# Optimization experiments

Measured on AMD Instinct MI355X. Metric: run time of the kernel, lower is better.

The kernel has to match this reference:

```python
import jax, jax.numpy as jnp
import numpy as np

B, CIN, T = 32, 1024, 600
NES, SCALE = 8, 8
CBLK = CIN // NES          # 128 channels per outer block
W = CBLK // SCALE          # 16 channels per scale branch
NIN = SCALE - 1            # 7 inner conv branches per Bottle2neck
NOUT = NES - 1             # 7 outer Bottle2neck blocks
NCLS = 2
EPS = 1e-5


def _bn1d(x, p):  # x:(B,C,T), p:(4,C) = gamma,beta,running_mean,running_var (inference BN)
    g, b, m, v = p
    return (x - m[:, None]) * (g[:, None] * jax.lax.rsqrt(v[:, None] + EPS)) + b[:, None]


def _bn2d(x, p):  # x:(B,C,T,S), p:(4,C)
    g, b, m, v = p
    r = lambda a: a[:, None, None]
    return (x - r(m)) * (r(g) * jax.lax.rsqrt(r(v) + EPS)) + r(b)


def _conv1x1(x, w, b):  # x:(B,C,T), w:(O,C), b:(O,)
    return jnp.einsum('oc,bct->bot', w, x) + b[:, None]


def _bottle2neck(x, w1, b1, bn1, cw, cb, ibn, ws, w3, b3, bn3, s1w, s1b, s2w, s2b):
    residual = x
    out = _bn1d(jax.nn.relu(_conv1x1(x, w1, b1)), bn1)[..., None]  # (B,128,T,1)
    spx = [out[:, i * W:(i + 1) * W] for i in range(SCALE)]
    sp = spx[NIN]
    outs = []
    for j in range(NIN):
        sp = jnp.concatenate([sp, spx[j]], axis=-1)                # (B,W,T,j+2)
        y = jax.lax.conv_general_dilated(
            sp, cw[j], window_strides=(1, 1), padding=((2, 2), (0, 0)),
            rhs_dilation=(2, 1), dimension_numbers=('NCHW', 'OIHW', 'NCHW'))
        y = y + cb[j][None, :, None, None]
        sp = _bn2d(jax.nn.relu(y), ibn[j])
        outs.append(jnp.sum(sp * ws[j][None, None, None, :], axis=-1))  # learnable weighted sum over scale dim
    outs.append(spx[NIN][..., 0])
    out = jnp.concatenate(outs, axis=1)                            # (B,128,T)
    out = _bn1d(jax.nn.relu(_conv1x1(out, w3, b3)), bn3)
    s = jnp.mean(out, axis=-1, keepdims=True)                      # SE squeeze
    s = jax.nn.relu(jnp.einsum('oc,bcx->box', s1w, s) + s1b[:, None])
    s = jax.nn.sigmoid(jnp.einsum('oc,bcx->box', s2w, s) + s2b[:, None])
    return out * s + residual


def _fwd(x, w1, b1, bn1, cw, cb, ibn, ws0, ws1, ws2, ws3, ws4, ws5, ws6,
         w3, b3, bn3, se1w, se1b, se2w, se2b, obn, fbn, fcw, fcb):
    wss = [ws0, ws1, ws2, ws3, ws4, ws5, ws6]
    spx = [x[:, i * CBLK:(i + 1) * CBLK] for i in range(NES)]
    sp = None
    outs = []
    for i in range(NOUT):
        sp = spx[i] if i == 0 else sp + spx[i]
        sp = _bottle2neck(sp, w1[i], b1[i], bn1[i], cw[i], cb[i], ibn[i],
                          [w[i] for w in wss], w3[i], b3[i], bn3[i],
                          se1w[i], se1b[i], se2w[i], se2b[i])
        sp = _bn1d(jax.nn.relu(sp), obn[i])
        outs.append(sp)
    outs.append(spx[-1])
    out = jax.nn.relu(_bn1d(jnp.concatenate(outs, axis=1), fbn))   # (B,1024,T)
    out = jnp.mean(out, axis=-1)                                   # mean pooling over time
    return out @ fcw.T + fcb                                       # (B,2)


def setup_inputs():
    key = jax.random.key(0)
    keys = iter(jax.random.split(key, 64))
    nrm = lambda shape, s=1.0: s * jax.random.normal(next(keys), shape, jnp.float32)

    def bn_params(shape):
        g = 1.0 + nrm(shape, 0.1)
        b = nrm(shape, 0.1)
        m = nrm(shape, 0.1)
        v = 0.5 + jax.random.uniform(next(keys), shape, jnp.float32)
        return jnp.stack([g, b, m, v], axis=-2)  # (..., 4, C)

    inp = {
        'x': nrm((B, CIN, T)),
        'w1': nrm((NOUT, CBLK, CBLK), CBLK ** -0.5), 'b1': nrm((NOUT, CBLK), 0.02),
        'bn1': bn_params((NOUT, CBLK)),
        'cw': nrm((NOUT, NIN, W, W, 3, 1), (W * 3) ** -0.5), 'cb': nrm((NOUT, NIN, W), 0.02),
        'ibn': bn_params((NOUT, NIN, W)),
        'w3': nrm((NOUT, CBLK, CBLK), CBLK ** -0.5), 'b3': nrm((NOUT, CBLK), 0.02),
        'bn3': bn_params((NOUT, CBLK)),
        'se1w': nrm((NOUT, CBLK // 8, CBLK), CBLK ** -0.5), 'se1b': nrm((NOUT, CBLK // 8), 0.02),
        'se2w': nrm((NOUT, CBLK, CBLK // 8), (CBLK // 8) ** -0.5), 'se2b': nrm((NOUT, CBLK), 0.02),
        'obn': bn_params((NOUT, CBLK)),
        'fbn': bn_params((CIN,)),
        'fcw': nrm((NCLS, CIN), CIN ** -0.5), 'fcb': nrm((NCLS,), 0.02),
    }
    for j in range(NIN):
        inp[f'ws{j}'] = jnp.full((NOUT, j + 2), 1.0 / (j + 2), jnp.float32)
    return inp


def reference(x, w1, b1, bn1, cw, cb, ibn, ws0, ws1, ws2, ws3, ws4, ws5, ws6,
              w3, b3, bn3, se1w, se1b, se2w, se2b, obn, fbn, fcw, fcb):
    return _fwd(x, w1, b1, bn1, cw, cb, ibn, ws0, ws1, ws2, ws3, ws4, ws5, ws6,
                w3, b3, bn3, se1w, se1b, se2w, se2b, obn, fbn, fcw, fcb)
```

## Files before the change

kernel.cpp:

```cpp
#include <hip/hip_runtime.h>
#include <hip/hip_bf16.h>

#define B_ 32
#define T_ 600

typedef __attribute__((ext_vector_type(8))) short short8;
typedef __attribute__((ext_vector_type(4))) float f32x4;
typedef __attribute__((ext_vector_type(4))) unsigned short ushort4v;

static __device__ __forceinline__ unsigned short f2bf(float f) {
    unsigned u = __float_as_uint(f);
    u += 0x7FFFu + ((u >> 16) & 1u);
    return (unsigned short)(u >> 16);
}
static __device__ __forceinline__ float bf2f(unsigned short u) {
    return __uint_as_float(((unsigned)u) << 16);
}

template<bool HAS_IN2, bool DO_SSUM, bool OUT_BF16>
__global__ __launch_bounds__(256) void gemm_kernel(
    const float* __restrict__ in0, int s0,
    const float* __restrict__ in1,
    const float* __restrict__ Wg, const float* __restrict__ bias,
    const float* __restrict__ bnp, void* __restrict__ outv,
    float* __restrict__ ssum,
    float* __restrict__ zbuf4096)
{
    __shared__ unsigned short Al[128][136];
    __shared__ unsigned short Bl[64][136];
    const int tid = threadIdx.x;
    const int b = blockIdx.y;
    const int t0 = blockIdx.x * 64;

    if (zbuf4096 != nullptr) {
        int fid = (b * gridDim.x + blockIdx.x) * 256 + tid;
        if (fid < 4096) zbuf4096[fid] = 0.f;
    }

    for (int e = tid; e < 128 * 32; e += 256) {
        int row = e >> 5, c4 = (e & 31) * 4;
        float4 w4 = *(const float4*)&Wg[row * 128 + c4];
        ushort4v u;
        u.x = f2bf(w4.x); u.y = f2bf(w4.y); u.z = f2bf(w4.z); u.w = f2bf(w4.w);
        *(ushort4v*)&Al[row][c4] = u;
    }
    {
        int t = tid & 63, cb = tid >> 6;
        int gt = t0 + t;
        bool inr = gt < T_;
        const float* p0 = in0 + b * s0 + gt;
        const float* p1 = HAS_IN2 ? (in1 + b * 614400 + gt) : nullptr;
        for (int q = 0; q < 32; q += 8) {
            unsigned short u8[8];
#pragma unroll
            for (int r = 0; r < 8; ++r) {
                int c = cb * 32 + q + r;
                float v = 0.f;
                if (inr) {
                    v = p0[c * T_];
                    if (HAS_IN2) v += p1[c * T_];
                }
                u8[r] = f2bf(v);
            }
            *(short8*)&Bl[t][cb * 32 + q] = *(short8*)u8;
        }
    }
    __syncthreads();

    const int wave = tid >> 6, lane = tid & 63;
    const int mBase = (wave >> 1) * 64, nBase = (wave & 1) * 32;
    const int lr = lane & 15, lq = lane >> 4;

    f32x4 acc[4][2];
#pragma unroll
    for (int mf = 0; mf < 4; ++mf)
#pragma unroll
        for (int nf = 0; nf < 2; ++nf) acc[mf][nf] = {0.f, 0.f, 0.f, 0.f};

#pragma unroll
    for (int kb = 0; kb < 4; ++kb) {
        short8 af[4], bfr[2];
#pragma unroll
        for (int mf = 0; mf < 4; ++mf)
            af[mf] = *(const short8*)&Al[mBase + mf * 16 + lr][kb * 32 + lq * 8];
#pragma unroll
        for (int nf = 0; nf < 2; ++nf)
            bfr[nf] = *(const short8*)&Bl[nBase + nf * 16 + lr][kb * 32 + lq * 8];
#pragma unroll
        for (int mf = 0; mf < 4; ++mf)
#pragma unroll
            for (int nf = 0; nf < 2; ++nf)
                acc[mf][nf] = __builtin_amdgcn_mfma_f32_16x16x32_bf16(
                    af[mf], bfr[nf], acc[mf][nf], 0, 0, 0);
    }

#pragma unroll
    for (int mf = 0; mf < 4; ++mf) {
#pragma unroll
        for (int i = 0; i < 4; ++i) {
            int o = mBase + mf * 16 + lq * 4 + i;
            float g = bnp[o], be = bnp[128 + o], m = bnp[256 + o], vv = bnp[384 + o];
            float sc = g * rsqrtf(vv + 1e-5f), sh = be - m * sc;
            float bs = bias[o];
            float psum = 0.f;
#pragma unroll
            for (int nf = 0; nf < 2; ++nf) {
                int t = t0 + nBase + nf * 16 + lr;
                float v = fmaxf(acc[mf][nf][i] + bs, 0.f) * sc + sh;
                if (t < T_) {
                    if (OUT_BF16)
                        ((unsigned short*)outv)[(b * 128 + o) * T_ + t] = f2bf(v);
                    else
                        ((float*)outv)[(b * 128 + o) * T_ + t] = v;
                    psum += v;
                }
            }
            if (DO_SSUM) {
                psum += __shfl_xor(psum, 1);
                psum += __shfl_xor(psum, 2);
                psum += __shfl_xor(psum, 4);
                psum += __shfl_xor(psum, 8);
                if (lr == 0) atomicAdd(&ssum[b * 128 + o], psum);
            }
        }
    }
}

constexpr int TI = 100;
constexpr int NROW = 132;
constexpr int RS = 24;

__global__ __launch_bounds__(128, 3) void inner_kernel(
    const unsigned short* __restrict__ out1, float* __restrict__ mid,
    unsigned short* __restrict__ chainout,
    const float* __restrict__ cwB, const float* __restrict__ cbB,
    const float* __restrict__ ibnB)
{
    __shared__ __attribute__((aligned(16))) unsigned short st[2][NROW][RS];
    __shared__ __attribute__((aligned(16))) unsigned short wL1[7 * 16 * 32];
    __shared__ __attribute__((aligned(16))) unsigned short wL2[7 * 16 * 16];
    __shared__ __attribute__((aligned(16))) unsigned short zb[16];
    __shared__ __attribute__((aligned(16))) float pL[7 * 16][4];

    const int tid = threadIdx.x;
    const int tile = blockIdx.x;
    const int c = blockIdx.y;
    const int b = blockIdx.z;

    const int j0 = (c <= 1) ? 0 : (c - 1);
    const int nconv = 7 - j0;
    const int halo = 2 * nconv;
    const int X = TI + 2 * halo;
    const int ch0 = (c == 0) ? 112 : 16 * (c - 1);
    const int t0g = tile * TI - halo;

    for (int e = tid; e < 2 * NROW * RS / 4; e += 128)
        ((ushort4v*)st)[e] = ushort4v{0, 0, 0, 0};
    if (tid < 16) zb[tid] = 0;

    for (int e = tid; e < nconv * 512; e += 128) {
        int k = e >> 9, rem = e & 511, o = rem >> 5, col = rem & 31;
        int tap = col >> 4, i = col & 15;
        wL1[e] = f2bf(cwB[((j0 + k) * 16 + o) * 48 + i * 3 + tap]);
    }
    for (int e = tid; e < nconv * 256; e += 128) {
        int k = e >> 8, rem = e & 255, o = rem >> 4, i = rem & 15;
        wL2[e] = f2bf(cwB[((j0 + k) * 16 + o) * 48 + i * 3 + 2]);
    }
    for (int e = tid; e < nconv * 16; e += 128) {
        int k = e >> 4, o = e & 15, j = j0 + k;
        float g = ibnB[(j * 4 + 0) * 16 + o], bb = ibnB[(j * 4 + 1) * 16 + o];
        float m = ibnB[(j * 4 + 2) * 16 + o], v = ibnB[(j * 4 + 3) * 16 + o];
        float sc = g * rsqrtf(v + 1e-5f);
        pL[e][0] = cbB[j * 16 + o];
        pL[e][1] = sc;
        pL[e][2] = bb - m * sc;
        pL[e][3] = 0.f;
    }
    __syncthreads();

    {
        const int i = tid >> 3, ph = tid & 7;
        const unsigned short* src = out1 + (size_t)(b * 128 + ch0 + i) * T_;
        for (int t = ph; t < X; t += 8) {
            int g = t0g + t;
            unsigned short v = ((unsigned)g < (unsigned)T_) ? src[g] : (unsigned short)0;
            st[0][t + 2][i] = v;
            if (c == 0 && t >= halo && t < halo + TI)
                mid[(size_t)(b * 128 + 112 + i) * T_ + g] = bf2f(v);
        }
    }
    __syncthreads();

    const int lane = tid & 63, wave = tid >> 6;
    const int lt = lane & 15, q = lane >> 4;
    const int i0 = (q & 1) * 8;
    const int roff1 = (q < 2) ? 0 : 2;

    int cur = 0;
    for (int k = 0; k < nconv; ++k) {
        const int olo = 2 * k + 2, ohi = X - 2 * k - 2;
        const int thi = (ohi + 15) >> 4;
        const int nxt = cur ^ 1;

        short8 A1 = *(const short8*)&wL1[(k * 16 + lt) * 32 + q * 8];
        short8 A2 = (q < 2)
            ? *(const short8*)&wL2[(k * 16 + lt) * 16 + q * 8]
            : *(const short8*)&zb[i0];
        float4 pp[4];
#pragma unroll
        for (int r = 0; r < 4; ++r)
            pp[r] = *(const float4*)&pL[k * 16 + 4 * q + r][0];

        for (int tt = wave; tt < thi; tt += 2) {
            const int t = tt * 16 + lt;
            f32x4 acc = {0.f, 0.f, 0.f, 0.f};
            short8 B1 = *(const short8*)&st[cur][t + roff1][i0];
            acc = __builtin_amdgcn_mfma_f32_16x16x32_bf16(A1, B1, acc, 0, 0, 0);
            short8 B2 = *(const short8*)&st[cur][t + 4][i0];
            acc = __builtin_amdgcn_mfma_f32_16x16x32_bf16(A2, B2, acc, 0, 0, 0);

            const int g = t0g + t;
            const bool ok = (t >= olo) && (t < ohi) && ((unsigned)g < (unsigned)T_);
            ushort4v o4;
#pragma unroll
            for (int r = 0; r < 4; ++r) {
                float v = fmaxf(acc[r] + pp[r].x, 0.f) * pp[r].y + pp[r].z;
                unsigned short h = f2bf(v);
                o4[r] = ok ? h : (unsigned short)0;
            }
            *(ushort4v*)&st[nxt][t + 2][4 * q] = o4;
        }
        __syncthreads();

        {
            const int j = j0 + k;
            const int pair = j * (j + 3) / 2 + c;
            unsigned short* dst = chainout + ((size_t)(pair * B_ + b) * 16) * T_
                                + tile * TI;
            const int i = tid >> 3, ph = tid & 7;
            for (int t2 = ph; t2 < TI; t2 += 8)
                dst[i * T_ + t2] = st[nxt][halo + t2 + 2][i];
        }
        cur = nxt;
    }
}

constexpr int WSUM_ITEMS = 7 * B_ * 16 * 75;

__global__ __launch_bounds__(256) void wsum_kernel(
    const unsigned short* __restrict__ chainout, float* __restrict__ mid,
    const float* __restrict__ ws0, const float* __restrict__ ws1,
    const float* __restrict__ ws2, const float* __restrict__ ws3,
    const float* __restrict__ ws4, const float* __restrict__ ws5,
    const float* __restrict__ ws6)
{
    int e = blockIdx.x * 256 + threadIdx.x;
    if (e >= WSUM_ITEMS) return;
    const int j = e / (B_ * 16 * 75);
    int r = e - j * (B_ * 16 * 75);
    const int b = r / (16 * 75);
    r -= b * (16 * 75);
    const int i = r / 75;
    const int tv = r - i * 75;

    const float* wp;
    switch (j) {
        case 0: wp = ws0; break; case 1: wp = ws1; break;
        case 2: wp = ws2; break; case 3: wp = ws3; break;
        case 4: wp = ws4; break; case 5: wp = ws5; break;
        default: wp = ws6; break;
    }
    const int nsl = j + 2, pair0 = j * (j + 3) / 2;
    const unsigned short* src = chainout + (size_t)(pair0 * B_ + b) * 9600
                              + i * T_ + tv * 8;
    float acc[8] = {0.f, 0.f, 0.f, 0.f, 0.f, 0.f, 0.f, 0.f};
    for (int s = 0; s < nsl; ++s) {
        short8 v = *(const short8*)(src + (size_t)s * B_ * 9600);
        float w = wp[s];
#pragma unroll
        for (int d = 0; d < 8; ++d)
            acc[d] += w * bf2f((unsigned short)v[d]);
    }
    float* dst = mid + (size_t)(b * 128 + 16 * j + i) * T_ + tv * 8;
    *(f32x4*)dst = {acc[0], acc[1], acc[2], acc[3]};
    *(f32x4*)(dst + 4) = {acc[4], acc[5], acc[6], acc[7]};
}

__global__ __launch_bounds__(128) void se_kernel(
    const float* __restrict__ ssum, const float* __restrict__ w1se,
    const float* __restrict__ b1se, const float* __restrict__ w2se,
    const float* __restrict__ b2se, float* __restrict__ s2b)
{
    __shared__ float sL[128], hL[16];
    const int tid = threadIdx.x, b = blockIdx.x;
    sL[tid] = ssum[b * 128 + tid] * (1.f / 600.f);
    __syncthreads();
    if (tid < 16) {
        float a = b1se[tid];
        for (int c = 0; c < 128; ++c) a += w1se[tid * 128 + c] * sL[c];
        hL[tid] = fmaxf(a, 0.f);
    }
    __syncthreads();
    float a = b2se[tid];
#pragma unroll
    for (int q = 0; q < 16; ++q) a += w2se[tid * 16 + q] * hL[q];
    s2b[b * 128 + tid] = 1.f / (1.f + expf(-a));
}

template<bool HAS_R2>
__global__ __launch_bounds__(256) void fuse_kernel(
    const float* __restrict__ out3, const float* __restrict__ s2b,
    const float* __restrict__ res0, int r0s,
    const float* __restrict__ res1,
    const float* __restrict__ obnp, const float* __restrict__ fbnp, int chOff,
    float* __restrict__ spOut, float* __restrict__ pooled)
{
    const int tid = threadIdx.x;
    const int row = blockIdx.x * 4 + (tid >> 6);
    const int lane = tid & 63;
    const int b = row >> 7, c = row & 127;
    const float s2v = s2b[b * 128 + c];
    float g = obnp[c], bb = obnp[128 + c], m = obnp[256 + c], v = obnp[384 + c];
    float osc = g * rsqrtf(v + 1e-5f), osh = bb - m * osc;
    int fc = chOff + c;
    float fg = fbnp[fc], fb2 = fbnp[1024 + fc], fm = fbnp[2048 + fc], fv = fbnp[3072 + fc];
    float fsc = fg * rsqrtf(fv + 1e-5f), fsh = fb2 - fm * fsc;
    int base = (b * 128 + c) * T_;
    float psum = 0.f;
    for (int t = lane; t < T_; t += 64) {
        float o3 = out3[base + t];
        float r = res0[b * r0s + c * T_ + t];
        if (HAS_R2) r += res1[b * 614400 + c * T_ + t];
        float fin = o3 * s2v + r;
        float sp = fmaxf(fin, 0.f) * osc + osh;
        spOut[base + t] = sp;
        psum += fmaxf(sp * fsc + fsh, 0.f);
    }
    for (int mo = 32; mo > 0; mo >>= 1) psum += __shfl_xor(psum, mo);
    if (lane == 0) pooled[b * 1024 + fc] = psum * (1.f / 600.f);
}

__global__ __launch_bounds__(256) void pooledx_kernel(
    const float* __restrict__ x, const float* __restrict__ fbnp,
    float* __restrict__ pooled)
{
    const int tid = threadIdx.x;
    const int row = blockIdx.x * 4 + (tid >> 6);
    const int lane = tid & 63;
    const int b = row >> 7, c = row & 127;
    int fc = 896 + c;
    float fg = fbnp[fc], fb2 = fbnp[1024 + fc], fm = fbnp[2048 + fc], fv = fbnp[3072 + fc];
    float fsc = fg * rsqrtf(fv + 1e-5f), fsh = fb2 - fm * fsc;
    int base = (b * 1024 + fc) * T_;
    float psum = 0.f;
    for (int t = lane; t < T_; t += 64)
        psum += fmaxf(x[base + t] * fsc + fsh, 0.f);
    for (int mo = 32; mo > 0; mo >>= 1) psum += __shfl_xor(psum, mo);
    if (lane == 0) pooled[b * 1024 + fc] = psum * (1.f / 600.f);
}

__global__ __launch_bounds__(256) void logits_kernel(
    const float* __restrict__ pooled, const float* __restrict__ fcw,
    const float* __restrict__ fcb, float* __restrict__ outp)
{
    __shared__ float red[256];
    const int tid = threadIdx.x;
    const int item = tid & 63, part = tid >> 6;
    const int b = item >> 1, cls = item & 1;
    float a = 0.f;
    for (int c = part * 256; c < part * 256 + 256; ++c)
        a += pooled[b * 1024 + c] * fcw[cls * 1024 + c];
    red[tid] = a;
    __syncthreads();
    if (tid < 64)
        outp[b * 2 + cls] = red[tid] + red[tid + 64] + red[tid + 128] + red[tid + 192] + fcb[cls];
}

extern "C" void kernel_launch(void* const* d_in, const int* in_sizes, int n_in,
                              void* d_out, int out_size, void* d_ws, size_t ws_size,
                              hipStream_t stream) {
    const float* x    = (const float*)d_in[0];
    const float* w1   = (const float*)d_in[1];
    const float* b1   = (const float*)d_in[2];
    const float* bn1  = (const float*)d_in[3];
    const float* cw   = (const float*)d_in[4];
    const float* cb   = (const float*)d_in[5];
    const float* ibn  = (const float*)d_in[6];
    const float* w3   = (const float*)d_in[7];
    const float* b3   = (const float*)d_in[8];
    const float* bn3  = (const float*)d_in[9];
    const float* se1w = (const float*)d_in[10];
    const float* se1b = (const float*)d_in[11];
    const float* se2w = (const float*)d_in[12];
    const float* se2b = (const float*)d_in[13];
    const float* obn  = (const float*)d_in[14];
    const float* fbn  = (const float*)d_in[15];
    const float* fcw  = (const float*)d_in[16];
    const float* fcb  = (const float*)d_in[17];
    const float* wsp[7] = {(const float*)d_in[18], (const float*)d_in[19],
                           (const float*)d_in[20], (const float*)d_in[21],
                           (const float*)d_in[22], (const float*)d_in[23],
                           (const float*)d_in[24]};

    float* ws = (float*)d_ws;
    const int NT = 128 * T_ * B_;
    unsigned short* out1h = (unsigned short*)ws;
    float* mid    = ws + NT;
    float* out3   = mid + NT;
    float* spA    = out3 + NT;
    float* spB    = spA + NT;
    float* sbuf   = spB + NT;
    float* s2b    = sbuf + 7 * 4096;
    float* pooled = s2b + 4096;
    unsigned short* chainout = (unsigned short*)(pooled + 32768);

    pooledx_kernel<<<1024, 256, 0, stream>>>(x, fbn, pooled);

    dim3 gGrid(10, B_);
    dim3 iGrid(6, 8, B_);
    const int wGrid = (WSUM_ITEMS + 255) / 256;

    float* spBufs[2] = {spA, spB};
    for (int i = 0; i < 7; ++i) {
        float* spOut = spBufs[i & 1];
        const float* spIn = spBufs[(i & 1) ^ 1];

        if (i == 0)
            gemm_kernel<false, false, true><<<gGrid, 256, 0, stream>>>(
                x, 614400, nullptr, w1, b1, bn1, out1h, nullptr,
                sbuf + i * 4096);
        else
            gemm_kernel<true, false, true><<<gGrid, 256, 0, stream>>>(
                spIn, 76800, x + i * 76800,
                w1 + i * 16384, b1 + i * 128, bn1 + i * 512, out1h, nullptr,
                sbuf + i * 4096);

        inner_kernel<<<iGrid, 128, 0, stream>>>(
            out1h, mid, chainout, cw + i * 5376, cb + i * 112, ibn + i * 448);

        wsum_kernel<<<wGrid, 256, 0, stream>>>(
            chainout, mid,
            wsp[0] + 2 * i, wsp[1] + 3 * i, wsp[2] + 4 * i, wsp[3] + 5 * i,
            wsp[4] + 6 * i, wsp[5] + 7 * i, wsp[6] + 8 * i);

        gemm_kernel<false, true, false><<<gGrid, 256, 0, stream>>>(
            mid, 76800, nullptr,
            w3 + i * 16384, b3 + i * 128, bn3 + i * 512, out3, sbuf + i * 4096,
            nullptr);

        se_kernel<<<B_, 128, 0, stream>>>(
            sbuf + i * 4096, se1w + i * 2048, se1b + i * 16,
            se2w + i * 2048, se2b + i * 128, s2b);

        if (i == 0)
            fuse_kernel<false><<<1024, 256, 0, stream>>>(
                out3, s2b, x, 614400, nullptr, obn, fbn, 0, spOut, pooled);
        else
            fuse_kernel<true><<<1024, 256, 0, stream>>>(
                out3, s2b, spIn, 76800, x + i * 76800,
                obn + i * 512, fbn, i * 128, spOut, pooled);
    }

    logits_kernel<<<1, 256, 0, stream>>>(pooled, fcw, fcb, (float*)d_out);
}
```

Baseline: 912.2 us.

## Fuse scale-weighted sum into conv3 GEMM and SE into fuse kernel; halve inner tile

The separate weighted-sum kernel and its fp32 'mid' buffer are removed. The second 1x1 GEMM now builds its B tile directly from the bf16 chain outputs, applying the learnable scale weights, and reads the passthrough channels from out1h. The SE excitation MLP moves into every fuse block, replacing the se_kernel launch, and the inner conv tile shrinks from 100 to 50 timesteps to double the grid. This cuts launches and global traffic but adds redundant SE compute per block, scattered strided loads in the GEMM prologue, and more halo recompute in the inner kernel.

```diff
diff --git a/kernel.cpp b/kernel.cpp
--- a/kernel.cpp
+++ b/kernel.cpp
@@ -17,13 +17,12 @@
     return __uint_as_float(((unsigned)u) << 16);
 }
 
-template<bool HAS_IN2, bool DO_SSUM, bool OUT_BF16>
+template<bool HAS_IN2>
 __global__ __launch_bounds__(256) void gemm_kernel(
     const float* __restrict__ in0, int s0,
     const float* __restrict__ in1,
     const float* __restrict__ Wg, const float* __restrict__ bias,
-    const float* __restrict__ bnp, void* __restrict__ outv,
-    float* __restrict__ ssum,
+    const float* __restrict__ bnp, unsigned short* __restrict__ out,
     float* __restrict__ zbuf4096)
 {
     __shared__ unsigned short Al[128][136];
@@ -102,36 +101,143 @@
             float g = bnp[o], be = bnp[128 + o], m = bnp[256 + o], vv = bnp[384 + o];
             float sc = g * rsqrtf(vv + 1e-5f), sh = be - m * sc;
             float bs = bias[o];
-            float psum = 0.f;
 #pragma unroll
             for (int nf = 0; nf < 2; ++nf) {
                 int t = t0 + nBase + nf * 16 + lr;
                 float v = fmaxf(acc[mf][nf][i] + bs, 0.f) * sc + sh;
-                if (t < T_) {
-                    if (OUT_BF16)
-                        ((unsigned short*)outv)[(b * 128 + o) * T_ + t] = f2bf(v);
-                    else
-                        ((float*)outv)[(b * 128 + o) * T_ + t] = v;
-                    psum += v;
+                if (t < T_) out[(b * 128 + o) * T_ + t] = f2bf(v);
+            }
+        }
+    }
+}
+
+__global__ __launch_bounds__(256) void gemm3_kernel(
+    const unsigned short* __restrict__ chainout,
+    const unsigned short* __restrict__ out1h,
+    const float* __restrict__ Wg, const float* __restrict__ bias,
+    const float* __restrict__ bnp, float* __restrict__ out,
+    float* __restrict__ ssum,
+    const float* __restrict__ ws0, const float* __restrict__ ws1,
+    const float* __restrict__ ws2, const float* __restrict__ ws3,
+    const float* __restrict__ ws4, const float* __restrict__ ws5,
+    const float* __restrict__ ws6)
+{
+    __shared__ unsigned short Al[128][136];
+    __shared__ unsigned short Bl[64][136];
+    __shared__ float wsL[7][8];
+    const int tid = threadIdx.x;
+    const int b = blockIdx.y;
+    const int t0 = blockIdx.x * 64;
+
+    if (tid < 56) {
+        int j = tid >> 3, s = tid & 7;
+        const float* wp;
+        switch (j) {
+            case 0: wp = ws0; break; case 1: wp = ws1; break;
+            case 2: wp = ws2; break; case 3: wp = ws3; break;
+            case 4: wp = ws4; break; case 5: wp = ws5; break;
+            default: wp = ws6; break;
+        }
+        wsL[j][s] = (s < j + 2) ? wp[s] : 0.f;
+    }
+    __syncthreads();
+
+    for (int e = tid; e < 128 * 32; e += 256) {
+        int row = e >> 5, c4 = (e & 31) * 4;
+        float4 w4 = *(const float4*)&Wg[row * 128 + c4];
+        ushort4v u;
+        u.x = f2bf(w4.x); u.y = f2bf(w4.y); u.z = f2bf(w4.z); u.w = f2bf(w4.w);
+        *(ushort4v*)&Al[row][c4] = u;
+    }
+    {
+        int t = tid & 63, cb = tid >> 6;
+        int gt = t0 + t;
+        bool inr = gt < T_;
+        for (int q = 0; q < 32; q += 8) {
+            unsigned short u8[8];
+#pragma unroll
+            for (int r = 0; r < 8; ++r) {
+                int c = cb * 32 + q + r;
+                float v = 0.f;
+                if (inr) {
+                    if (c < 112) {
+                        int j = c >> 4, i = c & 15;
+                        int pair0 = j * (j + 3) / 2;
+                        const unsigned short* src = chainout
+                            + ((size_t)(pair0 * B_ + b) * 16 + i) * T_ + gt;
+                        int nsl = j + 2;
+                        float a = 0.f;
+                        for (int s = 0; s < nsl; ++s)
+                            a += wsL[j][s] * bf2f(src[(size_t)s * B_ * 16 * T_]);
+                        v = a;
+                    } else {
+                        v = bf2f(out1h[((size_t)b * 128 + c) * T_ + gt]);
+                    }
                 }
+                u8[r] = f2bf(v);
             }
-            if (DO_SSUM) {
-                psum += __shfl_xor(psum, 1);
-                psum += __shfl_xor(psum, 2);
-                psum += __shfl_xor(psum, 4);
-                psum += __shfl_xor(psum, 8);
-                if (lr == 0) atomicAdd(&ssum[b * 128 + o], psum);
+            *(short8*)&Bl[t][cb * 32 + q] = *(short8*)u8;
+        }
+    }
+    __syncthreads();
+
+    const int wave = tid >> 6, lane = tid & 63;
+    const int mBase = (wave >> 1) * 64, nBase = (wave & 1) * 32;
+    const int lr = lane & 15, lq = lane >> 4;
+
+    f32x4 acc[4][2];
+#pragma unroll
+    for (int mf = 0; mf < 4; ++mf)
+#pragma unroll
+        for (int nf = 0; nf < 2; ++nf) acc[mf][nf] = {0.f, 0.f, 0.f, 0.f};
+
+#pragma unroll
+    for (int kb = 0; kb < 4; ++kb) {
+        short8 af[4], bfr[2];
+#pragma unroll
+        for (int mf = 0; mf < 4; ++mf)
+            af[mf] = *(const short8*)&Al[mBase + mf * 16 + lr][kb * 32 + lq * 8];
+#pragma unroll
+        for (int nf = 0; nf < 2; ++nf)
+            bfr[nf] = *(const short8*)&Bl[nBase + nf * 16 + lr][kb * 32 + lq * 8];
+#pragma unroll
+        for (int mf = 0; mf < 4; ++mf)
+#pragma unroll
+            for (int nf = 0; nf < 2; ++nf)
+                acc[mf][nf] = __builtin_amdgcn_mfma_f32_16x16x32_bf16(
+                    af[mf], bfr[nf], acc[mf][nf], 0, 0, 0);
+    }
+
+#pragma unroll
+    for (int mf = 0; mf < 4; ++mf) {
+#pragma unroll
+        for (int i = 0; i < 4; ++i) {
+            int o = mBase + mf * 16 + lq * 4 + i;
+            float g = bnp[o], be = bnp[128 + o], m = bnp[256 + o], vv = bnp[384 + o];
+            float sc = g * rsqrtf(vv + 1e-5f), sh = be - m * sc;
+            float bs = bias[o];
+            float psum = 0.f;
+#pragma unroll
+            for (int nf = 0; nf < 2; ++nf) {
+                int t = t0 + nBase + nf * 16 + lr;
+                float v = fmaxf(acc[mf][nf][i] + bs, 0.f) * sc + sh;
+                if (t < T_) { out[(b * 128 + o) * T_ + t] = v; psum += v; }
             }
-        }
-    }
-}
-
-constexpr int TI = 100;
-constexpr int NROW = 132;
+            psum += __shfl_xor(psum, 1);
+            psum += __shfl_xor(psum, 2);
+            psum += __shfl_xor(psum, 4);
+            psum += __shfl_xor(psum, 8);
+            if (lr == 0) atomicAdd(&ssum[b * 128 + o], psum);
+        }
+    }
+}
+
+constexpr int TI = 50;
+constexpr int NROW = 84;
 constexpr int RS = 24;
 
 __global__ __launch_bounds__(128, 3) void inner_kernel(
-    const unsigned short* __restrict__ out1, float* __restrict__ mid,
+    const unsigned short* __restrict__ out1,
     unsigned short* __restrict__ chainout,
     const float* __restrict__ cwB, const float* __restrict__ cbB,
     const float* __restrict__ ibnB)
@@ -184,10 +290,7 @@
         const unsigned short* src = out1 + (size_t)(b * 128 + ch0 + i) * T_;
         for (int t = ph; t < X; t += 8) {
             int g = t0g + t;
-            unsigned short v = ((unsigned)g < (unsigned)T_) ? src[g] : (unsigned short)0;
-            st[0][t + 2][i] = v;
-            if (c == 0 && t >= halo && t < halo + TI)
-                mid[(size_t)(b * 128 + 112 + i) * T_ + g] = bf2f(v);
+            st[0][t + 2][i] = ((unsigned)g < (unsigned)T_) ? src[g] : (unsigned short)0;
         }
     }
     __syncthreads();
@@ -246,81 +349,45 @@
     }
 }
 
-constexpr int WSUM_ITEMS = 7 * B_ * 16 * 75;
-
-__global__ __launch_bounds__(256) void wsum_kernel(
-    const unsigned short* __restrict__ chainout, float* __restrict__ mid,
-    const float* __restrict__ ws0, const float* __restrict__ ws1,
-    const float* __restrict__ ws2, const float* __restrict__ ws3,
-    const float* __restrict__ ws4, const float* __restrict__ ws5,
-    const float* __restrict__ ws6)
-{
-    int e = blockIdx.x * 256 + threadIdx.x;
-    if (e >= WSUM_ITEMS) return;
-    const int j = e / (B_ * 16 * 75);
-    int r = e - j * (B_ * 16 * 75);
-    const int b = r / (16 * 75);
-    r -= b * (16 * 75);
-    const int i = r / 75;
-    const int tv = r - i * 75;
-
-    const float* wp;
-    switch (j) {
-        case 0: wp = ws0; break; case 1: wp = ws1; break;
-        case 2: wp = ws2; break; case 3: wp = ws3; break;
-        case 4: wp = ws4; break; case 5: wp = ws5; break;
-        default: wp = ws6; break;
-    }
-    const int nsl = j + 2, pair0 = j * (j + 3) / 2;
-    const unsigned short* src = chainout + (size_t)(pair0 * B_ + b) * 9600
-                              + i * T_ + tv * 8;
-    float acc[8] = {0.f, 0.f, 0.f, 0.f, 0.f, 0.f, 0.f, 0.f};
-    for (int s = 0; s < nsl; ++s) {
-        short8 v = *(const short8*)(src + (size_t)s * B_ * 9600);
-        float w = wp[s];
-#pragma unroll
-        for (int d = 0; d < 8; ++d)
-            acc[d] += w * bf2f((unsigned short)v[d]);
-    }
-    float* dst = mid + (size_t)(b * 128 + 16 * j + i) * T_ + tv * 8;
-    *(f32x4*)dst = {acc[0], acc[1], acc[2], acc[3]};
-    *(f32x4*)(dst + 4) = {acc[4], acc[5], acc[6], acc[7]};
-}
-
-__global__ __launch_bounds__(128) void se_kernel(
-    const float* __restrict__ ssum, const float* __restrict__ w1se,
-    const float* __restrict__ b1se, const float* __restrict__ w2se,
-    const float* __restrict__ b2se, float* __restrict__ s2b)
-{
-    __shared__ float sL[128], hL[16];
-    const int tid = threadIdx.x, b = blockIdx.x;
-    sL[tid] = ssum[b * 128 + tid] * (1.f / 600.f);
-    __syncthreads();
-    if (tid < 16) {
-        float a = b1se[tid];
-        for (int c = 0; c < 128; ++c) a += w1se[tid * 128 + c] * sL[c];
-        hL[tid] = fmaxf(a, 0.f);
-    }
-    __syncthreads();
-    float a = b2se[tid];
-#pragma unroll
-    for (int q = 0; q < 16; ++q) a += w2se[tid * 16 + q] * hL[q];
-    s2b[b * 128 + tid] = 1.f / (1.f + expf(-a));
-}
-
 template<bool HAS_R2>
 __global__ __launch_bounds__(256) void fuse_kernel(
-    const float* __restrict__ out3, const float* __restrict__ s2b,
+    const float* __restrict__ out3, const float* __restrict__ ssum,
+    const float* __restrict__ w1se, const float* __restrict__ b1se,
+    const float* __restrict__ w2se, const float* __restrict__ b2se,
     const float* __restrict__ res0, int r0s,
     const float* __restrict__ res1,
     const float* __restrict__ obnp, const float* __restrict__ fbnp, int chOff,
     float* __restrict__ spOut, float* __restrict__ pooled)
 {
+    __shared__ float sL[128], red[128], hL[16];
     const int tid = threadIdx.x;
     const int row = blockIdx.x * 4 + (tid >> 6);
     const int lane = tid & 63;
     const int b = row >> 7, c = row & 127;
-    const float s2v = s2b[b * 128 + c];
+
+    if (tid < 128) sL[tid] = ssum[b * 128 + tid] * (1.f / 600.f);
+    __syncthreads();
+    if (tid < 128) {
+        int h = tid >> 3, part = tid & 7;
+        float a = 0.f;
+        const float* wrow = w1se + h * 128 + part * 16;
+#pragma unroll
+        for (int k = 0; k < 16; ++k) a += wrow[k] * sL[part * 16 + k];
+        red[tid] = a;
+    }
+    __syncthreads();
+    if (tid < 16) {
+        float a = b1se[tid];
+#pragma unroll
+        for (int p = 0; p < 8; ++p) a += red[tid * 8 + p];
+        hL[tid] = fmaxf(a, 0.f);
+    }
+    __syncthreads();
+    float a2 = b2se[c];
+#pragma unroll
+    for (int qq = 0; qq < 16; ++qq) a2 += w2se[c * 16 + qq] * hL[qq];
+    const float s2v = 1.f / (1.f + expf(-a2));
+
     float g = obnp[c], bb = obnp[128 + c], m = obnp[256 + c], v = obnp[384 + c];
     float osc = g * rsqrtf(v + 1e-5f), osh = bb - m * osc;
     int fc = chOff + c;
@@ -406,20 +473,17 @@
     float* ws = (float*)d_ws;
     const int NT = 128 * T_ * B_;
     unsigned short* out1h = (unsigned short*)ws;
-    float* mid    = ws + NT;
-    float* out3   = mid + NT;
+    float* out3   = ws + NT;
     float* spA    = out3 + NT;
     float* spB    = spA + NT;
     float* sbuf   = spB + NT;
-    float* s2b    = sbuf + 7 * 4096;
-    float* pooled = s2b + 4096;
+    float* pooled = sbuf + 7 * 4096;
     unsigned short* chainout = (unsigned short*)(pooled + 32768);
 
     pooledx_kernel<<<1024, 256, 0, stream>>>(x, fbn, pooled);
 
     dim3 gGrid(10, B_);
-    dim3 iGrid(6, 8, B_);
-    const int wGrid = (WSUM_ITEMS + 255) / 256;
+    dim3 iGrid(12, 8, B_);
 
     float* spBufs[2] = {spA, spB};
     for (int i = 0; i < 7; ++i) {
@@ -427,38 +491,32 @@
         const float* spIn = spBufs[(i & 1) ^ 1];
 
         if (i == 0)
-            gemm_kernel<false, false, true><<<gGrid, 256, 0, stream>>>(
-                x, 614400, nullptr, w1, b1, bn1, out1h, nullptr,
+            gemm_kernel<false><<<gGrid, 256, 0, stream>>>(
+                x, 614400, nullptr, w1, b1, bn1, out1h, sbuf + i * 4096);
+        else
+            gemm_kernel<true><<<gGrid, 256, 0, stream>>>(
+                spIn, 76800, x + i * 76800,
+                w1 + i * 16384, b1 + i * 128, bn1 + i * 512, out1h,
                 sbuf + i * 4096);
-        else
-            gemm_kernel<true, false, true><<<gGrid, 256, 0, stream>>>(
-                spIn, 76800, x + i * 76800,
-                w1 + i * 16384, b1 + i * 128, bn1 + i * 512, out1h, nullptr,
-                sbuf + i * 4096);
 
         inner_kernel<<<iGrid, 128, 0, stream>>>(
-            out1h, mid, chainout, cw + i * 5376, cb + i * 112, ibn + i * 448);
-
-        wsum_kernel<<<wGrid, 256, 0, stream>>>(
-            chainout, mid,
+            out1h, chainout, cw + i * 5376, cb + i * 112, ibn + i * 448);
+
+        gemm3_kernel<<<gGrid, 256, 0, stream>>>(
+            chainout, out1h,
+            w3 + i * 16384, b3 + i * 128, bn3 + i * 512, out3, sbuf + i * 4096,
             wsp[0] + 2 * i, wsp[1] + 3 * i, wsp[2] + 4 * i, wsp[3] + 5 * i,
             wsp[4] + 6 * i, wsp[5] + 7 * i, wsp[6] + 8 * i);
 
-        gemm_kernel<false, true, false><<<gGrid, 256, 0, stream>>>(
-            mid, 76800, nullptr,
-            w3 + i * 16384, b3 + i * 128, bn3 + i * 512, out3, sbuf + i * 4096,
-            nullptr);
-
-        se_kernel<<<B_, 128, 0, stream>>>(
-            sbuf + i * 4096, se1w + i * 2048, se1b + i * 16,
-            se2w + i * 2048, se2b + i * 128, s2b);
-
         if (i == 0)
             fuse_kernel<false><<<1024, 256, 0, stream>>>(
-                out3, s2b, x, 614400, nullptr, obn, fbn, 0, spOut, pooled);
+                out3, sbuf + i * 4096, se1w, se1b, se2w, se2b,
+                x, 614400, nullptr, obn, fbn, 0, spOut, pooled);
         else
             fuse_kernel<true><<<1024, 256, 0, stream>>>(
-                out3, s2b, spIn, 76800, x + i * 76800,
+                out3, sbuf + i * 4096,
+                se1w + i * 2048, se1b + i * 16, se2w + i * 2048, se2b + i * 128,
+                spIn, 76800, x + i * 76800,
                 obn + i * 512, fbn, i * 128, spOut, pooled);
     }
 
```

After: 1.168 ms. +28.1%, slower.
